# Performance work log

Measured on AMD Instinct MI355X. Metric: run time of the kernel, lower is better.

Reference implementation:

```python
import jax, jax.numpy as jnp
import numpy as np

B, T, DIM, HEADS = 4, 2048, 1024, 16
D_K = DIM // HEADS


def setup_inputs() -> dict:
    key = jax.random.key(0)
    ks = jax.random.split(key, 5)
    x = jax.random.normal(ks[0], (B, T, DIM), dtype=jnp.float32)
    # nn.Linear params: weight [out, in], bias [out]
    w_qkv = jax.random.normal(ks[1], (3 * DIM, DIM), dtype=jnp.float32) / np.sqrt(DIM)
    b_qkv = jax.random.normal(ks[2], (3 * DIM,), dtype=jnp.float32) * 0.02
    w_out = jax.random.normal(ks[3], (DIM, DIM), dtype=jnp.float32) / np.sqrt(DIM)
    b_out = jax.random.normal(ks[4], (DIM,), dtype=jnp.float32) * 0.02
    # causal mask, broadcast over batch and heads: [1, 1, T, T]
    mask = jnp.tril(jnp.ones((T, T), dtype=jnp.int32))[None, None]
    return {"x": x, "w_qkv": w_qkv, "b_qkv": b_qkv, "w_out": w_out, "b_out": b_out, "mask": mask}


def reference(x, w_qkv, b_qkv, w_out, b_out, mask):
    Bb, Tt, D = x.shape
    # fused QKV projection: [B,T,3D] -> [3,B,H,T,d_k]
    qkv = (x @ w_qkv.T + b_qkv).reshape(Bb, Tt, 3, HEADS, D_K).transpose(2, 0, 3, 1, 4)
    q, k, v = qkv[0], qkv[1], qkv[2]
    scores = jnp.einsum("bhqd,bhkd->bhqk", q, k) / jnp.sqrt(jnp.float32(D_K))
    scores = jnp.where(mask == 0, -jnp.inf, scores)
    attn = jax.nn.softmax(scores, axis=-1)  # [B,H,T,T]
    context = jnp.einsum("bhqk,bhkd->bhqd", attn, v)
    context = context.transpose(0, 2, 1, 3).reshape(Bb, Tt, D)
    return context @ w_out.T + b_out
```

## Files before the change

### kernel.cpp

```cpp
#include <hip/hip_runtime.h>

typedef unsigned short ushort_t;
typedef __bf16 bf16x8 __attribute__((ext_vector_type(8)));
typedef float f32x4 __attribute__((ext_vector_type(4)));

#define BB 4
#define TT 2048
#define DIMD 1024
#define NH 16
#define DK 64
#define MROWS (BB * TT)
#define NQKV (3 * DIMD)

__device__ __forceinline__ ushort_t f2b(float f) {
  __bf16 h = (__bf16)f;
  union { __bf16 h; ushort_t u; } c; c.h = h; return c.u;
}

__device__ __forceinline__ void gload_lds16(const void* g, void* l) {
  __builtin_amdgcn_global_load_lds(
      (const __attribute__((address_space(1))) void*)g,
      (__attribute__((address_space(3))) void*)l,
      16, 0, 0);
}

__global__ __launch_bounds__(256) void cast_f32_bf16(
    const float* __restrict__ in, ushort_t* __restrict__ out, int n)
{
  const int i = (blockIdx.x * 256 + threadIdx.x) * 8;
  if (i >= n) return;
  float4 a = *(const float4*)(in + i);
  float4 b = *(const float4*)(in + i + 4);
  ushort_t o[8];
  o[0] = f2b(a.x); o[1] = f2b(a.y); o[2] = f2b(a.z); o[3] = f2b(a.w);
  o[4] = f2b(b.x); o[5] = f2b(b.y); o[6] = f2b(b.z); o[7] = f2b(b.w);
  *(uint4*)(out + i) = *(const uint4*)o;
}

template <bool OUT_F32>
__global__ __launch_bounds__(256) void gemm_bt_bias(
    const ushort_t* __restrict__ A, const ushort_t* __restrict__ W,
    const float* __restrict__ bias, void* __restrict__ Cp,
    int M, int N, int K)
{
  __shared__ __align__(16) ushort_t As[128 * 32];
  __shared__ __align__(16) ushort_t Bs[128 * 32];

  const int tid = threadIdx.x;
  const int wave = tid >> 6, lane = tid & 63;
  const int tiles_n = N >> 7;
  const int bm = blockIdx.x / tiles_n, bn = blockIdx.x % tiles_n;
  const int row0 = bm << 7, col0 = bn << 7;
  const int wm = (wave >> 1) << 6;
  const int wn = (wave & 1) << 6;
  const int fr = lane & 15;
  const int fk = (lane >> 4) << 3;
  const int g4 = (lane >> 4) << 2;

  const int sr = lane >> 2;
  const int csw = fk ^ (((fr >> 1) & 3) << 3);

  f32x4 acc[4][4] = {};

  for (int k0 = 0; k0 < K; k0 += 32) {
    __syncthreads();
#pragma unroll
    for (int p = 0; p < 2; ++p) {
      const int e = (wave << 9) + (p << 11);
      const int r = (e >> 5) + sr;
      const int c = ((lane & 3) << 3) ^ (((r >> 1) & 3) << 3);
      gload_lds16(A + (size_t)(row0 + r) * K + (k0 + c), As + e);
      gload_lds16(W + (size_t)(col0 + r) * K + (k0 + c), Bs + e);
    }
    __syncthreads();

    bf16x8 af[4], bw[4];
#pragma unroll
    for (int i = 0; i < 4; ++i) {
      af[i] = *(const bf16x8*)&As[(wm + (i << 4) + fr) * 32 + csw];
      bw[i] = *(const bf16x8*)&Bs[(wn + (i << 4) + fr) * 32 + csw];
    }
#pragma unroll
    for (int mi = 0; mi < 4; ++mi)
#pragma unroll
      for (int ni = 0; ni < 4; ++ni)
        acc[mi][ni] = __builtin_amdgcn_mfma_f32_16x16x32_bf16(af[mi], bw[ni], acc[mi][ni], 0, 0, 0);
  }

#pragma unroll
  for (int ni = 0; ni < 4; ++ni) {
    const int col = col0 + wn + (ni << 4) + fr;
    const float bv = bias[col];
#pragma unroll
    for (int mi = 0; mi < 4; ++mi)
#pragma unroll
      for (int r = 0; r < 4; ++r) {
        const size_t row = (size_t)(row0 + wm + (mi << 4) + g4 + r);
        if constexpr (OUT_F32)
          ((float*)Cp)[row * (size_t)N + col] = acc[mi][ni][r] + bv;
        else
          ((ushort_t*)Cp)[row * (size_t)N + col] = f2b(acc[mi][ni][r] + bv);
      }
  }
}

__global__ __launch_bounds__(512, 4) void attn_fused(
    const ushort_t* __restrict__ qkv, ushort_t* __restrict__ ctx)
{
  __shared__ __align__(16) ushort_t Qs[128 * 64];
  __shared__ __align__(16) ushort_t Ks[2][64 * 64];
  __shared__ __align__(16) ushort_t Vt[64 * 64];
  __shared__ __align__(16) ushort_t Ps[8][16 * 64];

  const int tid = threadIdx.x, wave = tid >> 6, lane = tid & 63;
  const int fr = lane & 15;
  const int g  = lane >> 4;
  const int fk = g << 3;
  const int g4 = g << 2;

  const int bid = blockIdx.x;
  const int bq  = (bid >> 3) & 7;
  const int G   = (bid & 7) | ((bid >> 6) << 3);
  const int h   = G & 15;
  const int b   = G >> 4;

  const int srl = lane >> 3;
  const int scc = ((lane & 7) ^ srl) << 3;
  const int vr  = tid >> 3;
  const int vc  = (tid & 7) << 3;
  const int rsw = (fr & 7) << 3;

  const ushort_t* Kg = qkv + (size_t)b * TT * NQKV + DIMD + h * DK;
  const ushort_t* Vg = qkv + (size_t)b * TT * NQKV + 2 * DIMD + h * DK;

#pragma unroll 1
  for (int t = 0; t < 2; ++t) {
    const int qt = t ? (15 - bq) : bq;
    const int ktmax = 2 * qt + 1;
    const size_t qrow0 = (size_t)b * TT + (size_t)qt * 128;

    __syncthreads();

    const ushort_t* Qg = qkv + qrow0 * NQKV + h * DK;
#pragma unroll
    for (int pp = 0; pp < 2; ++pp) {
      const int e  = (wave << 9) + (pp << 12);
      const int rr = (e >> 6) + srl;
      gload_lds16(Qg + (size_t)rr * NQKV + scc, Qs + e);
    }
    {
      const int e  = wave << 9;
      const int rr = (wave << 3) + srl;
      gload_lds16(Kg + (size_t)rr * NQKV + scc, Ks[0] + e);
    }
    uint4 va = *(const uint4*)(Vg + (size_t)vr * NQKV + vc);
    asm volatile("s_waitcnt vmcnt(0)" ::: "memory");
    __syncthreads();

    bf16x8 aqr[2];
#pragma unroll
    for (int ks = 0; ks < 2; ++ks)
      aqr[ks] = *(const bf16x8*)&Qs[((wave << 4) + fr) * 64 + (((ks << 5) + fk) ^ rsw)];

    const int qrow = (qt << 7) + (wave << 4) + fr;
    float mrow = -1e30f, lrow = 0.f;
    f32x4 oacc[4] = {};
    int cur = 0;

    for (int kt = 0; kt <= ktmax; ++kt) {
      {
        __align__(16) ushort_t tmp[8];
        *(uint4*)tmp = va;
#pragma unroll
        for (int j = 0; j < 8; ++j) {
          const int d  = vc + j;
          const int hh = (d & 7) ^ ((d >> 3) & 7);
          Vt[d * 64 + (vr ^ (hh << 3))] = tmp[j];
        }
      }
      if (kt < ktmax) {
        const size_t krow = (size_t)(kt + 1) << 6;
        const int e  = wave << 9;
        const int rr = (wave << 3) + srl;
        gload_lds16(Kg + (krow + rr) * NQKV + scc, Ks[cur ^ 1] + e);
        va = *(const uint4*)(Vg + (krow + vr) * NQKV + vc);
      }
      asm volatile("s_waitcnt lgkmcnt(0)" ::: "memory");
      __builtin_amdgcn_s_barrier();

      f32x4 s[4] = {};
#pragma unroll
      for (int ks = 0; ks < 2; ++ks)
#pragma unroll
        for (int ni = 0; ni < 4; ++ni) {
          const bf16x8 bk = *(const bf16x8*)&Ks[cur][((ni << 4) + fr) * 64 + (((ks << 5) + fk) ^ rsw)];
          s[ni] = __builtin_amdgcn_mfma_f32_16x16x32_bf16(bk, aqr[ks], s[ni], 0, 0, 0);
        }

      const int kb = kt << 6;
#pragma unroll
      for (int ni = 0; ni < 4; ++ni)
#pragma unroll
        for (int r = 0; r < 4; ++r) {
          const int kc = kb + (ni << 4) + g4 + r;
          if (kc > qrow) s[ni][r] = -1e30f;
        }

      float rm = -1e30f;
#pragma unroll
      for (int ni = 0; ni < 4; ++ni) {
        const float m01 = fmaxf(s[ni][0], s[ni][1]);
        const float m23 = fmaxf(s[ni][2], s[ni][3]);
        rm = fmaxf(rm, fmaxf(m01, m23));
      }
      rm = fmaxf(rm, __shfl_xor(rm, 16, 64));
      rm = fmaxf(rm, __shfl_xor(rm, 32, 64));

      if (__any(rm > mrow + 64.f)) {
        const float mn = fmaxf(mrow, rm);
        const float corr = __expf((mrow - mn) * 0.125f);
        mrow = mn;
        lrow *= corr;
#pragma unroll
        for (int ni = 0; ni < 4; ++ni) oacc[ni] *= corr;
      }
      const float nm = -mrow * 0.125f;
      float rs = 0.f;
#pragma unroll
      for (int ni = 0; ni < 4; ++ni)
#pragma unroll
        for (int r = 0; r < 4; ++r) {
          const float pe = __expf(fmaf(s[ni][r], 0.125f, nm));
          s[ni][r] = pe;
          rs += pe;
        }
      rs += __shfl_xor(rs, 16, 64);
      rs += __shfl_xor(rs, 32, 64);
      lrow += rs;

#pragma unroll
      for (int ni = 0; ni < 4; ++ni) {
        ushort_t o4[4];
#pragma unroll
        for (int r = 0; r < 4; ++r) o4[r] = f2b(s[ni][r]);
        *(uint2*)&Ps[wave][fr * 64 + (((ni << 4) + g4) ^ rsw)] = *(const uint2*)o4;
      }
      asm volatile("s_waitcnt lgkmcnt(0)" ::: "memory");
      __builtin_amdgcn_sched_barrier(0);

#pragma unroll
      for (int ks = 0; ks < 2; ++ks) {
        const bf16x8 ap = *(const bf16x8*)&Ps[wave][fr * 64 + (((ks << 5) + fk) ^ rsw)];
#pragma unroll
        for (int ni = 0; ni < 4; ++ni) {
          const int hh = (fr & 7) ^ ((2 * ni + (fr >> 3)) & 7);
          const bf16x8 bv = *(const bf16x8*)&Vt[((ni << 4) + fr) * 64 + (((ks << 5) + fk) ^ (hh << 3))];
          oacc[ni] = __builtin_amdgcn_mfma_f32_16x16x32_bf16(bv, ap, oacc[ni], 0, 0, 0);
        }
      }

      if (kt < ktmax) {
        asm volatile("s_waitcnt vmcnt(0)" ::: "memory");
        __syncthreads();
      }
      cur ^= 1;
    }

    const float inv = 1.f / lrow;
    ushort_t* crow = ctx + (qrow0 + (wave << 4) + fr) * DIMD + h * DK;
#pragma unroll
    for (int ni = 0; ni < 4; ++ni) {
      ushort_t o4[4];
#pragma unroll
      for (int r = 0; r < 4; ++r) o4[r] = f2b(oacc[ni][r] * inv);
      *(uint2*)&crow[(ni << 4) + g4] = *(const uint2*)o4;
    }
  }
}

__global__ __launch_bounds__(256) void copy_f32(
    const float* __restrict__ in, float* __restrict__ out, int n)
{
  const int stride = gridDim.x * blockDim.x * 4;
  for (int i = (blockIdx.x * blockDim.x + threadIdx.x) * 4; i < n; i += stride)
    *(float4*)(out + i) = *(const float4*)(in + i);
}

extern "C" void kernel_launch(void* const* d_in, const int* in_sizes, int n_in,
                              void* d_out, int out_size, void* d_ws, size_t ws_size,
                              hipStream_t stream) {
  const float* x     = (const float*)d_in[0];
  const float* w_qkv = (const float*)d_in[1];
  const float* b_qkv = (const float*)d_in[2];
  const float* w_out = (const float*)d_in[3];
  const float* b_out = (const float*)d_in[4];

  const size_t need = (size_t)MROWS * NQKV * sizeof(ushort_t);
  if (ws_size < need) return;

  ushort_t* dsc  = (ushort_t*)d_out;
  ushort_t* xb   = dsc;
  ushort_t* wqb  = dsc + (size_t)MROWS * DIMD;
  ushort_t* wob  = wqb + (size_t)NQKV * DIMD;
  ushort_t* ctx  = dsc;

  ushort_t* qkv     = (ushort_t*)d_ws;
  float*    out_tmp = (float*)d_ws;
  float*    out     = (float*)d_out;

  cast_f32_bf16<<<dim3(MROWS * DIMD / 2048), dim3(256), 0, stream>>>(x, xb, MROWS * DIMD);
  cast_f32_bf16<<<dim3(NQKV * DIMD / 2048), dim3(256), 0, stream>>>(w_qkv, wqb, NQKV * DIMD);
  cast_f32_bf16<<<dim3(DIMD * DIMD / 2048), dim3(256), 0, stream>>>(w_out, wob, DIMD * DIMD);
  gemm_bt_bias<false><<<dim3((MROWS / 128) * (NQKV / 128)), dim3(256), 0, stream>>>(
      xb, wqb, b_qkv, (void*)qkv, MROWS, NQKV, DIMD);
  attn_fused<<<dim3(BB * NH * 8), dim3(512), 0, stream>>>(qkv, ctx);
  gemm_bt_bias<true><<<dim3((MROWS / 128) * (DIMD / 128)), dim3(256), 0, stream>>>(
      ctx, wob, b_out, (void*)out_tmp, MROWS, DIMD, DIMD);
  copy_f32<<<dim3(2048), dim3(256), 0, stream>>>(out_tmp, out, MROWS * DIMD);
}
```

Measured before the change: 202.9 us.

## Skip fully-masked attention tiles, use raw exp2, and drop output copy kernel

```diff
diff --git a/kernel.cpp b/kernel.cpp
--- a/kernel.cpp
+++ b/kernel.cpp
@@ -15,6 +15,11 @@
 __device__ __forceinline__ ushort_t f2b(float f) {
   __bf16 h = (__bf16)f;
   union { __bf16 h; ushort_t u; } c; c.h = h; return c.u;
+}
+__device__ __forceinline__ float fexp2(float x) {
+  float r;
+  asm("v_exp_f32 %0, %1" : "=v"(r) : "v"(x));
+  return r;
 }
 
 __device__ __forceinline__ void gload_lds16(const void* g, void* l) {
@@ -104,6 +109,7 @@
   }
 }
 
+#define C1 0.18033688011112042f
 __global__ __launch_bounds__(512, 4) void attn_fused(
     const ushort_t* __restrict__ qkv, ushort_t* __restrict__ ctx)
 {
@@ -137,6 +143,7 @@
   for (int t = 0; t < 2; ++t) {
     const int qt = t ? (15 - bq) : bq;
     const int ktmax = 2 * qt + 1;
+    const int diag  = 2 * qt + (wave >> 2);
     const size_t qrow0 = (size_t)b * TT + (size_t)qt * 128;
 
     __syncthreads();
@@ -188,75 +195,83 @@
       asm volatile("s_waitcnt lgkmcnt(0)" ::: "memory");
       __builtin_amdgcn_s_barrier();
 
-      f32x4 s[4] = {};
-#pragma unroll
-      for (int ks = 0; ks < 2; ++ks)
+      if (kt <= diag) {
+        f32x4 s[4] = {};
+        __builtin_amdgcn_s_setprio(1);
+#pragma unroll
+        for (int ks = 0; ks < 2; ++ks)
+#pragma unroll
+          for (int ni = 0; ni < 4; ++ni) {
+            const bf16x8 bk = *(const bf16x8*)&Ks[cur][((ni << 4) + fr) * 64 + (((ks << 5) + fk) ^ rsw)];
+            s[ni] = __builtin_amdgcn_mfma_f32_16x16x32_bf16(bk, aqr[ks], s[ni], 0, 0, 0);
+          }
+        __builtin_amdgcn_s_setprio(0);
+
+        if (kt == diag) {
+          const int kb = kt << 6;
+#pragma unroll
+          for (int ni = 0; ni < 4; ++ni)
+#pragma unroll
+            for (int r = 0; r < 4; ++r) {
+              const int kc = kb + (ni << 4) + g4 + r;
+              if (kc > qrow) s[ni][r] = -1e30f;
+            }
+        }
+
+        float rm = -1e30f;
 #pragma unroll
         for (int ni = 0; ni < 4; ++ni) {
-          const bf16x8 bk = *(const bf16x8*)&Ks[cur][((ni << 4) + fr) * 64 + (((ks << 5) + fk) ^ rsw)];
-          s[ni] = __builtin_amdgcn_mfma_f32_16x16x32_bf16(bk, aqr[ks], s[ni], 0, 0, 0);
-        }
-
-      const int kb = kt << 6;
-#pragma unroll
-      for (int ni = 0; ni < 4; ++ni)
-#pragma unroll
-        for (int r = 0; r < 4; ++r) {
-          const int kc = kb + (ni << 4) + g4 + r;
-          if (kc > qrow) s[ni][r] = -1e30f;
-        }
-
-      float rm = -1e30f;
-#pragma unroll
-      for (int ni = 0; ni < 4; ++ni) {
-        const float m01 = fmaxf(s[ni][0], s[ni][1]);
-        const float m23 = fmaxf(s[ni][2], s[ni][3]);
-        rm = fmaxf(rm, fmaxf(m01, m23));
-      }
-      rm = fmaxf(rm, __shfl_xor(rm, 16, 64));
-      rm = fmaxf(rm, __shfl_xor(rm, 32, 64));
-
-      if (__any(rm > mrow + 64.f)) {
-        const float mn = fmaxf(mrow, rm);
-        const float corr = __expf((mrow - mn) * 0.125f);
-        mrow = mn;
-        lrow *= corr;
-#pragma unroll
-        for (int ni = 0; ni < 4; ++ni) oacc[ni] *= corr;
-      }
-      const float nm = -mrow * 0.125f;
-      float rs = 0.f;
-#pragma unroll
-      for (int ni = 0; ni < 4; ++ni)
-#pragma unroll
-        for (int r = 0; r < 4; ++r) {
-          const float pe = __expf(fmaf(s[ni][r], 0.125f, nm));
-          s[ni][r] = pe;
-          rs += pe;
-        }
-      rs += __shfl_xor(rs, 16, 64);
-      rs += __shfl_xor(rs, 32, 64);
-      lrow += rs;
-
-#pragma unroll
-      for (int ni = 0; ni < 4; ++ni) {
-        ushort_t o4[4];
-#pragma unroll
-        for (int r = 0; r < 4; ++r) o4[r] = f2b(s[ni][r]);
-        *(uint2*)&Ps[wave][fr * 64 + (((ni << 4) + g4) ^ rsw)] = *(const uint2*)o4;
-      }
-      asm volatile("s_waitcnt lgkmcnt(0)" ::: "memory");
-      __builtin_amdgcn_sched_barrier(0);
-
-#pragma unroll
-      for (int ks = 0; ks < 2; ++ks) {
-        const bf16x8 ap = *(const bf16x8*)&Ps[wave][fr * 64 + (((ks << 5) + fk) ^ rsw)];
+          const float m01 = fmaxf(s[ni][0], s[ni][1]);
+          const float m23 = fmaxf(s[ni][2], s[ni][3]);
+          rm = fmaxf(rm, fmaxf(m01, m23));
+        }
+        rm = fmaxf(rm, __shfl_xor(rm, 16, 64));
+        rm = fmaxf(rm, __shfl_xor(rm, 32, 64));
+
+        if (__any(rm > mrow + 64.f)) {
+          const float mn = fmaxf(mrow, rm);
+          const float corr = fexp2((mrow - mn) * C1);
+          mrow = mn;
+          lrow *= corr;
+#pragma unroll
+          for (int ni = 0; ni < 4; ++ni) oacc[ni] *= corr;
+        }
+        const float nm2 = -mrow * C1;
+        float rs = 0.f;
+#pragma unroll
+        for (int ni = 0; ni < 4; ++ni)
+#pragma unroll
+          for (int r = 0; r < 4; ++r) {
+            const float pe = fexp2(fmaf(s[ni][r], C1, nm2));
+            s[ni][r] = pe;
+            rs += pe;
+          }
+        rs += __shfl_xor(rs, 16, 64);
+        rs += __shfl_xor(rs, 32, 64);
+        lrow += rs;
+
 #pragma unroll
         for (int ni = 0; ni < 4; ++ni) {
-          const int hh = (fr & 7) ^ ((2 * ni + (fr >> 3)) & 7);
-          const bf16x8 bv = *(const bf16x8*)&Vt[((ni << 4) + fr) * 64 + (((ks << 5) + fk) ^ (hh << 3))];
-          oacc[ni] = __builtin_amdgcn_mfma_f32_16x16x32_bf16(bv, ap, oacc[ni], 0, 0, 0);
-        }
+          ushort_t o4[4];
+#pragma unroll
+          for (int r = 0; r < 4; ++r) o4[r] = f2b(s[ni][r]);
+          *(uint2*)&Ps[wave][fr * 64 + (((ni << 4) + g4) ^ rsw)] = *(const uint2*)o4;
+        }
+        asm volatile("s_waitcnt lgkmcnt(0)" ::: "memory");
+        __builtin_amdgcn_sched_barrier(0);
+
+        __builtin_amdgcn_s_setprio(1);
+#pragma unroll
+        for (int ks = 0; ks < 2; ++ks) {
+          const bf16x8 ap = *(const bf16x8*)&Ps[wave][fr * 64 + (((ks << 5) + fk) ^ rsw)];
+#pragma unroll
+          for (int ni = 0; ni < 4; ++ni) {
+            const int hh = (fr & 7) ^ ((2 * ni + (fr >> 3)) & 7);
+            const bf16x8 bv = *(const bf16x8*)&Vt[((ni << 4) + fr) * 64 + (((ks << 5) + fk) ^ (hh << 3))];
+            oacc[ni] = __builtin_amdgcn_mfma_f32_16x16x32_bf16(bv, ap, oacc[ni], 0, 0, 0);
+          }
+        }
+        __builtin_amdgcn_s_setprio(0);
       }
 
       if (kt < ktmax) {
@@ -276,14 +291,6 @@
       *(uint2*)&crow[(ni << 4) + g4] = *(const uint2*)o4;
     }
   }
-}
-
-__global__ __launch_bounds__(256) void copy_f32(
-    const float* __restrict__ in, float* __restrict__ out, int n)
-{
-  const int stride = gridDim.x * blockDim.x * 4;
-  for (int i = (blockIdx.x * blockDim.x + threadIdx.x) * 4; i < n; i += stride)
-    *(float4*)(out + i) = *(const float4*)(in + i);
 }
 
 extern "C" void kernel_launch(void* const* d_in, const int* in_sizes, int n_in,
@@ -295,18 +302,15 @@
   const float* w_out = (const float*)d_in[3];
   const float* b_out = (const float*)d_in[4];
 
-  const size_t need = (size_t)MROWS * NQKV * sizeof(ushort_t);
+  const size_t need = 36u * 1024 * 1024 * sizeof(ushort_t);
   if (ws_size < need) return;
 
-  ushort_t* dsc  = (ushort_t*)d_out;
-  ushort_t* xb   = dsc;
-  ushort_t* wqb  = dsc + (size_t)MROWS * DIMD;
-  ushort_t* wob  = wqb + (size_t)NQKV * DIMD;
-  ushort_t* ctx  = dsc;
-
-  ushort_t* qkv     = (ushort_t*)d_ws;
-  float*    out_tmp = (float*)d_ws;
-  float*    out     = (float*)d_out;
+  ushort_t* qkv = (ushort_t*)d_ws;
+  ushort_t* xb  = qkv + (size_t)MROWS * NQKV;
+  ushort_t* wqb = xb  + (size_t)MROWS * DIMD;
+  ushort_t* wob = wqb + (size_t)NQKV * DIMD;
+  ushort_t* ctx = xb;
+  float*    out = (float*)d_out;
 
   cast_f32_bf16<<<dim3(MROWS * DIMD / 2048), dim3(256), 0, stream>>>(x, xb, MROWS * DIMD);
   cast_f32_bf16<<<dim3(NQKV * DIMD / 2048), dim3(256), 0, stream>>>(w_qkv, wqb, NQKV * DIMD);
@@ -315,6 +319,5 @@
       xb, wqb, b_qkv, (void*)qkv, MROWS, NQKV, DIMD);
   attn_fused<<<dim3(BB * NH * 8), dim3(512), 0, stream>>>(qkv, ctx);
   gemm_bt_bias<true><<<dim3((MROWS / 128) * (DIMD / 128)), dim3(256), 0, stream>>>(
-      ctx, wob, b_out, (void*)out_tmp, MROWS, DIMD, DIMD);
-  copy_f32<<<dim3(2048), dim3(256), 0, stream>>>(out_tmp, out, MROWS * DIMD);
-}
+      ctx, wob, b_out, (void*)out, MROWS, DIMD, DIMD);
+}
```

Measured after the change: 184.5 us. 1.1x faster.
